# Kernel optimization log

Measured on AMD Instinct MI355X. Metric: run time of the kernel, lower is better.

## Reference

```python
import jax, jax.numpy as jnp
import numpy as np

HIDDEN = 32
PAD = 2


def setup_inputs() -> dict:
    key = jax.random.key(0)
    ks = jax.random.split(key, 7)
    B, C, D, H, W = 4, 256, 32, 64, 64
    x = jax.random.normal(ks[0], (B, C, D, H, W), dtype=jnp.float32)
    # PyTorch LSTMCell params: W_ih (4H, in=1), W_hh (4H, H), biases (4H,)
    s_ih = 1.0 / np.sqrt(HIDDEN)
    W_ih = jax.random.uniform(ks[1], (4 * HIDDEN, 1), jnp.float32, -s_ih, s_ih)
    W_hh = jax.random.uniform(ks[2], (4 * HIDDEN, HIDDEN), jnp.float32, -s_ih, s_ih)
    b_ih = jax.random.uniform(ks[3], (4 * HIDDEN,), jnp.float32, -s_ih, s_ih)
    b_hh = jax.random.uniform(ks[4], (4 * HIDDEN,), jnp.float32, -s_ih, s_ih)
    gate_w = jax.random.uniform(ks[5], (1, HIDDEN), jnp.float32, -s_ih, s_ih)
    gate_b = jax.random.uniform(ks[6], (1,), jnp.float32, -s_ih, s_ih)
    return {"x": x, "W_ih": W_ih, "W_hh": W_hh, "b_ih": b_ih, "b_hh": b_hh,
            "gate_w": gate_w, "gate_b": gate_b}


def reference(x, W_ih, W_hh, b_ih, b_hh, gate_w, gate_b):
    B, C, D, H, W = x.shape
    p = PAD
    # ReflectionPad3d on spatial dims
    xp = jnp.pad(x, ((0, 0), (0, 0), (p, p), (p, p), (p, p)), mode="reflect")
    # per-channel spatial mean over the PADDED volume -> (B, C)
    channel_seq = xp.reshape(B, C, -1).mean(axis=2)
    bias = b_ih + b_hh  # (4H,)

    def step(carry, inp_t):  # inp_t: (B,) scalar channel feature per batch
        h, c = carry
        # gates: (B, 4H); input_size=1 so W_ih contributes inp * W_ih[:,0]
        z = inp_t[:, None] * W_ih[:, 0][None, :] + h @ W_hh.T + bias
        i, f, g, o = jnp.split(z, 4, axis=1)  # PyTorch i,f,g,o ordering
        c = jax.nn.sigmoid(f) * c + jax.nn.sigmoid(i) * jnp.tanh(g)
        h = jax.nn.sigmoid(o) * jnp.tanh(c)
        return (h, c), h

    h0 = jnp.zeros((B, HIDDEN), x.dtype)
    c0 = jnp.zeros((B, HIDDEN), x.dtype)
    _, hs = jax.lax.scan(step, (h0, c0), channel_seq.T)  # hs: (C, B, H)
    seq_outputs = hs.transpose(1, 0, 2)  # (B, C, H)
    # AlphaDropout is identity in eval mode
    gates = jax.nn.sigmoid(seq_outputs @ gate_w[0] + gate_b[0])  # (B, C)
    # reweight padded map then crop == reweight original x (reflect-pad crop is exact)
    return x * gates[:, :, None, None, None]
```

## Files before the change

kernel.cpp:

```cpp
#include <hip/hip_runtime.h>


#define CH_F4 32768
#define NCH 1024
#define MEAN_DEN (1.0f / 166464.0f)

__device__ __forceinline__ float sigf(float x) {
    return 1.0f / (1.0f + __expf(-x));
}
__device__ __forceinline__ float tanh_fast(float x) {
    return fmaf(2.0f, sigf(2.0f * x), -1.0f);
}

__global__ __launch_bounds__(256) void mean_kernel(const float* __restrict__ x,
                                                   float* __restrict__ cseq) {
    const int bc = blockIdx.x;
    const float4* __restrict__ p = (const float4*)x + (size_t)bc * CH_F4;
    const int tid = threadIdx.x;

    float sum = 0.0f;
    for (int i = tid; i < CH_F4; i += 256) {
        float4 v = p[i];
        const int q = i & 15;
        const int h = (i >> 4) & 63;
        const int d = i >> 10;
        float t = (v.x + v.y) + (v.z + v.w);
        if (q == 0 || q == 15) t += v.y + v.z;
        const float wd = ((d == 1) | (d == 2) | (d == 29) | (d == 30)) ? 2.0f : 1.0f;
        const float wh = ((h == 1) | (h == 2) | (h == 61) | (h == 62)) ? 2.0f : 1.0f;
        sum = fmaf(wd * wh, t, sum);
    }

    __shared__ float red[256];
    red[tid] = sum;
    __syncthreads();
    for (int s = 128; s > 0; s >>= 1) {
        if (tid < s) red[tid] += red[tid + s];
        __syncthreads();
    }
    if (tid == 0) cseq[bc] = red[0] * MEAN_DEN;
}

__global__ __launch_bounds__(64) void lstm_kernel(const float* __restrict__ cseq,
                                                  const float* __restrict__ W_ih,
                                                  const float* __restrict__ W_hh,
                                                  const float* __restrict__ b_ih,
                                                  const float* __restrict__ b_hh,
                                                  const float* __restrict__ gate_w,
                                                  const float* __restrict__ gate_b,
                                                  float* __restrict__ gates) {
    __shared__ float cs[256];
    __shared__ float hist[256 * 33 + 32];

    const int b = blockIdx.x;
    const int l = threadIdx.x;
    const int r0 = l, r1 = l + 64;

    const float wih0 = W_ih[r0];
    const float wih1 = W_ih[r1];
    const float bias0 = b_ih[r0] + b_hh[r0];
    const float bias1 = b_ih[r1] + b_hh[r1];
    float whh0[32], whh1[32];
#pragma unroll
    for (int k = 0; k < 32; k++) {
        whh0[k] = W_hh[r0 * 32 + k];
        whh1[k] = W_hh[r1 * 32 + k];
    }
#pragma unroll
    for (int i = 0; i < 4; i++) cs[l * 4 + i] = cseq[b * 256 + l * 4 + i];
    if (l < 32) hist[l] = 0.0f;
    float c = 0.0f;
    __syncthreads();

    for (int t = 0; t < 256; t++) {
        const float inp = cs[t];
        const float* hrow = &hist[t * 33];
        float z0 = fmaf(inp, wih0, bias0);
        float z1 = fmaf(inp, wih1, bias1);
#pragma unroll
        for (int k = 0; k < 32; k++) {
            const float hk = hrow[k];
            z0 = fmaf(hk, whh0[k], z0);
            z1 = fmaf(hk, whh1[k], z1);
        }
        const float zf = __shfl_xor(z0, 32);
        const float zo = __shfl_xor(z1, 32);
        c = sigf(zf) * c + sigf(z0) * tanh_fast(z1);
        const float hv = sigf(zo) * tanh_fast(c);
        if (l < 32) hist[(t + 1) * 33 + l] = hv;
        __syncthreads();
    }

    float gw[32];
#pragma unroll
    for (int k = 0; k < 32; k++) gw[k] = gate_w[k];
    const float gb = gate_b[0];
#pragma unroll
    for (int chunk = 0; chunk < 4; chunk++) {
        const int t = chunk * 64 + l;
        const float* hrow = &hist[(t + 1) * 33];
        float s = gb;
#pragma unroll
        for (int k = 0; k < 32; k++) s = fmaf(hrow[k], gw[k], s);
        gates[b * 256 + t] = sigf(s);
    }
}

__global__ __launch_bounds__(256) void scale_kernel(const float* __restrict__ x,
                                                    const float* __restrict__ gates,
                                                    float* __restrict__ out) {
    const int bc = (NCH - 1) - blockIdx.y;
    const float g = gates[bc];
    const size_t base = (size_t)bc * CH_F4;
    const float4* __restrict__ xi = (const float4*)x + base;
    float4* __restrict__ oi = (float4*)out + base;
    const int start = blockIdx.x * 1024 + threadIdx.x;
#pragma unroll
    for (int r = 0; r < 4; r++) {
        const int idx = start + r * 256;
        float4 v = xi[idx];
        v.x *= g; v.y *= g; v.z *= g; v.w *= g;
        oi[idx] = v;
    }
}

extern "C" void kernel_launch(void* const* d_in, const int* in_sizes, int n_in,
                              void* d_out, int out_size, void* d_ws, size_t ws_size,
                              hipStream_t stream) {
    const float* x      = (const float*)d_in[0];
    const float* W_ih   = (const float*)d_in[1];
    const float* W_hh   = (const float*)d_in[2];
    const float* b_ih   = (const float*)d_in[3];
    const float* b_hh   = (const float*)d_in[4];
    const float* gate_w = (const float*)d_in[5];
    const float* gate_b = (const float*)d_in[6];
    float* out = (float*)d_out;

    float* cseq  = (float*)d_ws;
    float* gates = (float*)d_ws + 1024;

    mean_kernel<<<NCH, 256, 0, stream>>>(x, cseq);
    lstm_kernel<<<4, 64, 0, stream>>>(cseq, W_ih, W_hh, b_ih, b_hh,
                                      gate_w, gate_b, gates);
    scale_kernel<<<dim3(32, NCH), 256, 0, stream>>>(x, gates, out);
}
```

Baseline: 417.1 us.

## Keep LSTM hidden state in registers via readlane, drop per-step barriers

The LSTM recurrence now broadcasts the hidden state across lanes with readlane instead of going through shared memory. This removes the __syncthreads from each of the 256 sequential steps, and the hidden history is still written to LDS for the final gate projection. The gate exchange uses permlane32_swap when the builtin is available. The scale kernel switches to native vector types with nontemporal stores to avoid polluting the cache with output. The LSTM change targets the serial latency-bound kernel; the scale kernel change is a minor bandwidth tweak.

```diff
diff --git a/kernel.cpp b/kernel.cpp
--- a/kernel.cpp
+++ b/kernel.cpp
@@ -4,6 +4,9 @@
 #define CH_F4 32768
 #define NCH 1024
 #define MEAN_DEN (1.0f / 166464.0f)
+
+typedef unsigned int uint;
+typedef float f32x4 __attribute__((ext_vector_type(4)));
 
 __device__ __forceinline__ float sigf(float x) {
     return 1.0f / (1.0f + __expf(-x));
@@ -15,12 +18,12 @@
 __global__ __launch_bounds__(256) void mean_kernel(const float* __restrict__ x,
                                                    float* __restrict__ cseq) {
     const int bc = blockIdx.x;
-    const float4* __restrict__ p = (const float4*)x + (size_t)bc * CH_F4;
+    const f32x4* __restrict__ p = (const f32x4*)x + (size_t)bc * CH_F4;
     const int tid = threadIdx.x;
 
     float sum = 0.0f;
     for (int i = tid; i < CH_F4; i += 256) {
-        float4 v = p[i];
+        f32x4 v = p[i];
         const int q = i & 15;
         const int h = (i >> 4) & 63;
         const int d = i >> 10;
@@ -50,7 +53,7 @@
                                                   const float* __restrict__ gate_b,
                                                   float* __restrict__ gates) {
     __shared__ float cs[256];
-    __shared__ float hist[256 * 33 + 32];
+    __shared__ float hist[257 * 33];
 
     const int b = blockIdx.x;
     const int l = threadIdx.x;
@@ -67,29 +70,41 @@
         whh1[k] = W_hh[r1 * 32 + k];
     }
 #pragma unroll
-    for (int i = 0; i < 4; i++) cs[l * 4 + i] = cseq[b * 256 + l * 4 + i];
-    if (l < 32) hist[l] = 0.0f;
+    for (int i = 0; i < 4; i++) cs[i * 64 + l] = cseq[b * 256 + i * 64 + l];
+    float h = 0.0f;
     float c = 0.0f;
     __syncthreads();
 
     for (int t = 0; t < 256; t++) {
         const float inp = cs[t];
-        const float* hrow = &hist[t * 33];
         float z0 = fmaf(inp, wih0, bias0);
         float z1 = fmaf(inp, wih1, bias1);
 #pragma unroll
         for (int k = 0; k < 32; k++) {
-            const float hk = hrow[k];
+            const float hk = __builtin_bit_cast(float,
+                __builtin_amdgcn_readlane(__builtin_bit_cast(int, h), k));
             z0 = fmaf(hk, whh0[k], z0);
             z1 = fmaf(hk, whh1[k], z1);
         }
-        const float zf = __shfl_xor(z0, 32);
-        const float zo = __shfl_xor(z1, 32);
+        float zf, zo;
+#if __has_builtin(__builtin_amdgcn_permlane32_swap)
+        {
+            auto ra = __builtin_amdgcn_permlane32_swap(
+                __builtin_bit_cast(uint, z0), __builtin_bit_cast(uint, z0), false, false);
+            auto rb = __builtin_amdgcn_permlane32_swap(
+                __builtin_bit_cast(uint, z1), __builtin_bit_cast(uint, z1), false, false);
+            zf = __builtin_bit_cast(float, ra[1]);
+            zo = __builtin_bit_cast(float, rb[1]);
+        }
+#else
+        zf = __shfl_xor(z0, 32);
+        zo = __shfl_xor(z1, 32);
+#endif
         c = sigf(zf) * c + sigf(z0) * tanh_fast(z1);
-        const float hv = sigf(zo) * tanh_fast(c);
-        if (l < 32) hist[(t + 1) * 33 + l] = hv;
-        __syncthreads();
+        h = sigf(zo) * tanh_fast(c);
+        if (l < 32) hist[(t + 1) * 33 + l] = h;
     }
+    __syncthreads();
 
     float gw[32];
 #pragma unroll
@@ -112,15 +127,15 @@
     const int bc = (NCH - 1) - blockIdx.y;
     const float g = gates[bc];
     const size_t base = (size_t)bc * CH_F4;
-    const float4* __restrict__ xi = (const float4*)x + base;
-    float4* __restrict__ oi = (float4*)out + base;
+    const f32x4* __restrict__ xi = (const f32x4*)x + base;
+    f32x4* __restrict__ oi = (f32x4*)out + base;
     const int start = blockIdx.x * 1024 + threadIdx.x;
 #pragma unroll
     for (int r = 0; r < 4; r++) {
         const int idx = start + r * 256;
-        float4 v = xi[idx];
-        v.x *= g; v.y *= g; v.z *= g; v.w *= g;
-        oi[idx] = v;
+        f32x4 v = xi[idx];
+        v *= g;
+        __builtin_nontemporal_store(v, &oi[idx]);
     }
 }
 
```

Measured after the change: 406.1 us. 2.6% less time.
